# Kernel optimization log

Hardware: AMD Instinct MI355X
Metric: run time of the kernel (lower is better)

Reference implementation:

```python
import jax, jax.numpy as jnp
import numpy as np

CE_W, BOUND_W, DICE_W, SMOOTH = 1.0, 0.1, 1.0, 1e-6


def setup_inputs() -> dict:
    key = jax.random.key(0)
    k1, k2 = jax.random.split(key)
    B, C, H, W = 8, 1, 256, 256
    logits = jax.random.normal(k1, (B, C, H, W), dtype=jnp.float32)
    target = jax.random.uniform(k2, (B, C, H, W), dtype=jnp.float32)
    return {"logits": logits, "target": target}


def _edt(fg):
    # fg: [B, H, W] bool foreground mask. Returns exact Euclidean distance
    # transform of the background (0 at foreground), matching
    # scipy.ndimage.distance_transform_edt(1 - fg).
    B, H, W = fg.shape
    INF = jnp.float32(H + W)  # larger than any in-image 1D distance

    # --- pass 1: vertical distance to nearest foreground in each column ---
    fg_t = jnp.transpose(fg, (1, 0, 2))  # [H, B, W], scan over rows

    def step(carry, fg_row):
        d = jnp.where(fg_row, 0.0, carry + 1.0)
        return d, d

    init = jnp.full((B, W), INF, dtype=jnp.float32)
    _, g_fwd = jax.lax.scan(step, init, fg_t)                 # top-down
    _, g_bwd = jax.lax.scan(step, init, fg_t, reverse=True)   # bottom-up
    g = jnp.minimum(g_fwd, g_bwd)          # [H, B, W]
    g = jnp.transpose(g, (1, 0, 2))        # [B, H, W]

    # --- pass 2: exact squared EDT per row: min_k (j-k)^2 + g[i,k]^2 ---
    j = jnp.arange(W, dtype=jnp.float32)
    offs2 = (j[:, None] - j[None, :]) ** 2                    # [W, W]
    # [B, H, Wj, Wk] intermediate -> min over k
    dt2 = jnp.min(g[:, :, None, :] ** 2 + offs2[None, None, :, :], axis=-1)
    dt = jnp.sqrt(dt2)

    # empty masks get an all-zero distance map (scipy branch in the original)
    nonempty = jnp.any(fg, axis=(1, 2))
    return jnp.where(nonempty[:, None, None], dt, 0.0)


def reference(logits, target):
    target = jnp.clip(target.astype(jnp.float32), 0.0, 1.0)

    # BCEWithLogitsLoss (mean): stable log(1 + e^x) - x*t
    ce = jnp.mean(jnp.logaddexp(0.0, logits) - logits * target)

    probs = jnp.clip(jax.nn.sigmoid(logits), SMOOTH, 1.0 - SMOOTH)

    # Dice over flattened tensors
    p, t = probs.reshape(-1), target.reshape(-1)
    inter = jnp.sum(p * t)
    dice = 1.0 - (2.0 * inter + SMOOTH) / (jnp.sum(p) + jnp.sum(t) + SMOOTH)

    # Boundary: mean(probs * EDT(target > 0.5)) -- EDT is non-differentiable data
    fg = target[:, 0] > 0.5                      # [B, H, W]
    dt = jax.lax.stop_gradient(_edt(fg))[:, None]  # [B, 1, H, W]
    boundary = jnp.mean(probs * dt)

    total = CE_W * ce + DICE_W * dice + BOUND_W * boundary
    return total, ce, dice, boundary
```

## Files before the change

### kernel.cpp

```cpp
#include <hip/hip_runtime.h>

#define BB 8
#define HH 256
#define WW 256
#define NROWS (BB * HH)
#define NTOT (BB * HH * WW)

__global__ __launch_bounds__(256) void build_masks(
    const float* __restrict__ target, unsigned* __restrict__ masks) {
  const int s = blockIdx.x;
  const int b = blockIdx.y;
  const int j = threadIdx.x;
  const float* base = target + b * (HH * WW) + s * 32 * WW + j;
  unsigned m = 0;
#pragma unroll
  for (int r = 0; r < 32; ++r)
    if (base[r * WW] > 0.5f) m |= (1u << r);
  masks[b * 2048 + s * 256 + j] = m;
}

__global__ __launch_bounds__(256) void main_kernel(
    const float* __restrict__ logits, const float* __restrict__ target,
    const unsigned* __restrict__ masks,
    float* __restrict__ partials ) {
  __shared__ float s_g2[WW];
  __shared__ float s_red[4 * 5];
  __shared__ int s_any[4];
  __shared__ int s_rmax[4];

  const int row = blockIdx.x;
  const int b = row >> 8;
  const int i = row & 255;
  const int j = threadIdx.x;
  const int rowbase = row * WW;
  const int lane = j & 63;
  const int wave = j >> 6;

  unsigned m[8];
#pragma unroll
  for (int w = 0; w < 8; ++w) m[w] = masks[b * 2048 + w * 256 + j];

  const int wi = i >> 5, r = i & 31;
  int dUp = 1 << 30, dDn = 1 << 30;
  const unsigned cur = m[wi] >> r;
  if (cur) {
    dUp = __builtin_ctz(cur);
  } else {
    int off = 32 - r;
    for (int w2 = wi + 1; w2 < 8; ++w2, off += 32)
      if (m[w2]) { dUp = off + __builtin_ctz(m[w2]); break; }
  }
  const unsigned curd = m[wi] << (31 - r);
  if (curd) {
    dDn = __builtin_clz(curd);
  } else {
    int off = r + 1;
    for (int w2 = wi - 1; w2 >= 0; --w2, off += 32)
      if (m[w2]) { dDn = off + __builtin_clz(m[w2]); break; }
  }
  const int d = min(dUp, dDn);
  s_g2[j] = (d < 256) ? (float)(d * d) : 1.0e9f;
  const int rj = min(d, 255);

  const unsigned many = m[0] | m[1] | m[2] | m[3] | m[4] | m[5] | m[6] | m[7];
  const int wave_any = __any(many != 0u);
  int rmax = rj;
#pragma unroll
  for (int off = 32; off > 0; off >>= 1) rmax = max(rmax, __shfl_down(rmax, off, 64));
  if (lane == 0) { s_any[wave] = wave_any; s_rmax[wave] = rmax; }
  __syncthreads();
  const int nonempty = s_any[0] | s_any[1] | s_any[2] | s_any[3];
  const int R = max(max(s_rmax[0], s_rmax[1]), max(s_rmax[2], s_rmax[3]));

  float mn = 1.0e30f;
  for (int dlt = -R; dlt <= R; ++dlt) {
    const int k = j + dlt;
    if ((unsigned)k < 256u)
      mn = fminf(mn, (float)(dlt * dlt) + s_g2[k]);
  }
  const float dt = nonempty ? sqrtf(mn) : 0.0f;

  const float x = logits[rowbase + j];
  float t = target[rowbase + j];
  t = fminf(fmaxf(t, 0.0f), 1.0f);
  const float e = __expf(-fabsf(x));
  const float inv = 1.0f / (1.0f + e);
  const float ce = fmaxf(x, 0.0f) + __logf(1.0f + e) - x * t;
  float p = (x >= 0.0f) ? inv : e * inv;
  p = fminf(fmaxf(p, 1e-6f), 1.0f - 1e-6f);

  float v[5];
  v[0] = ce;
  v[1] = p;
  v[2] = t;
  v[3] = p * t;
  v[4] = p * dt;

#pragma unroll
  for (int q = 0; q < 5; ++q) {
    float s = v[q];
#pragma unroll
    for (int off = 32; off > 0; off >>= 1) s += __shfl_down(s, off, 64);
    if (lane == 0) s_red[wave * 5 + q] = s;
  }
  __syncthreads();
  if (j == 0) {
#pragma unroll
    for (int q = 0; q < 5; ++q) {
      const float s = s_red[q] + s_red[5 + q] + s_red[10 + q] + s_red[15 + q];
      partials[q * NROWS + row] = s;
    }
  }
}

__global__ __launch_bounds__(256) void finalize(
    const float* __restrict__ partials, float* __restrict__ out) {
  __shared__ double s_red[4 * 5];
  const int j = threadIdx.x;
  double acc[5] = {0.0, 0.0, 0.0, 0.0, 0.0};
  for (int i = j; i < NROWS; i += 256) {
#pragma unroll
    for (int q = 0; q < 5; ++q) acc[q] += (double)partials[q * NROWS + i];
  }
  const int lane = j & 63;
  const int wave = j >> 6;
#pragma unroll
  for (int q = 0; q < 5; ++q) {
    double s = acc[q];
#pragma unroll
    for (int off = 32; off > 0; off >>= 1) s += __shfl_down(s, off, 64);
    if (lane == 0) s_red[wave * 5 + q] = s;
  }
  __syncthreads();
  if (j == 0) {
    double sum[5];
#pragma unroll
    for (int q = 0; q < 5; ++q)
      sum[q] = s_red[q] + s_red[5 + q] + s_red[10 + q] + s_red[15 + q];
    const double n = (double)NTOT;
    const double ce = sum[0] / n;
    const double dice = 1.0 - (2.0 * sum[3] + 1e-6) / (sum[1] + sum[2] + 1e-6);
    const double boundary = sum[4] / n;
    const double total = 1.0 * ce + 1.0 * dice + 0.1 * boundary;
    out[0] = (float)total;
    out[1] = (float)ce;
    out[2] = (float)dice;
    out[3] = (float)boundary;
  }
}

extern "C" void kernel_launch(void* const* d_in, const int* in_sizes, int n_in,
                              void* d_out, int out_size, void* d_ws,
                              size_t ws_size, hipStream_t stream) {
  const float* logits = (const float*)d_in[0];
  const float* target = (const float*)d_in[1];
  float* out = (float*)d_out;

  char* ws = (char*)d_ws;
  unsigned* masks = (unsigned*)ws;
  float* partials = (float*)(ws + 64 * 1024);

  build_masks<<<dim3(8, 8), 256, 0, stream>>>(target, masks);
  main_kernel<<<NROWS, 256, 0, stream>>>(logits, target, masks, partials);
  finalize<<<1, 256, 0, stream>>>(partials, out);
}
```

Measured before the change: 69.09 us.

## Process four rows per block and fuse finalize via atomic last-block reduction

Each block now handles four rows of the same image, so the eight mask words are loaded once per four rows and the block-level reductions and syncs are amortised. The separate finalize kernel is removed: blocks atomically add double partials into a workspace accumulator and the last-arriving block computes the outputs. This saves a kernel launch and the partials round trip, but adds double atomics contention and makes the EDT search radius R the maximum over four rows.

```diff
diff --git a/kernel.cpp b/kernel.cpp
--- a/kernel.cpp
+++ b/kernel.cpp
@@ -3,14 +3,26 @@
 #define BB 8
 #define HH 256
 #define WW 256
-#define NROWS (BB * HH)
 #define NTOT (BB * HH * WW)
+#define RPB 4
+#define NBLK (BB * HH / RPB)
+
+struct Accum {
+  double s[5];
+  unsigned int count;
+};
 
 __global__ __launch_bounds__(256) void build_masks(
-    const float* __restrict__ target, unsigned* __restrict__ masks) {
+    const float* __restrict__ target, unsigned* __restrict__ masks,
+    Accum* __restrict__ acc) {
   const int s = blockIdx.x;
   const int b = blockIdx.y;
   const int j = threadIdx.x;
+  if (s == 0 && b == 0 && j == 0) {
+#pragma unroll
+    for (int q = 0; q < 5; ++q) acc->s[q] = 0.0;
+    acc->count = 0u;
+  }
   const float* base = target + b * (HH * WW) + s * 32 * WW + j;
   unsigned m = 0;
 #pragma unroll
@@ -21,81 +33,83 @@
 
 __global__ __launch_bounds__(256) void main_kernel(
     const float* __restrict__ logits, const float* __restrict__ target,
-    const unsigned* __restrict__ masks,
-    float* __restrict__ partials ) {
-  __shared__ float s_g2[WW];
+    const unsigned* __restrict__ masks, Accum* __restrict__ acc,
+    float* __restrict__ out) {
+  __shared__ float s_g2[RPB][WW];
   __shared__ float s_red[4 * 5];
-  __shared__ int s_any[4];
-  __shared__ int s_rmax[4];
+  __shared__ int s_im[4 * 2];
 
-  const int row = blockIdx.x;
-  const int b = row >> 8;
-  const int i = row & 255;
+  const int g = blockIdx.x;
+  const int b = g >> 6;
+  const int i0 = (g & 63) * RPB;
   const int j = threadIdx.x;
-  const int rowbase = row * WW;
-  const int lane = j & 63;
-  const int wave = j >> 6;
+  const int lane = j & 63, wave = j >> 6;
 
   unsigned m[8];
 #pragma unroll
   for (int w = 0; w < 8; ++w) m[w] = masks[b * 2048 + w * 256 + j];
+  const unsigned many = m[0] | m[1] | m[2] | m[3] | m[4] | m[5] | m[6] | m[7];
 
-  const int wi = i >> 5, r = i & 31;
-  int dUp = 1 << 30, dDn = 1 << 30;
-  const unsigned cur = m[wi] >> r;
-  if (cur) {
-    dUp = __builtin_ctz(cur);
-  } else {
-    int off = 32 - r;
-    for (int w2 = wi + 1; w2 < 8; ++w2, off += 32)
-      if (m[w2]) { dUp = off + __builtin_ctz(m[w2]); break; }
+  int rmax = 0;
+#pragma unroll
+  for (int r = 0; r < RPB; ++r) {
+    const int i = i0 + r;
+    const int wi = i >> 5, rr = i & 31;
+    int dUp = 1 << 30, dDn = 1 << 30;
+    const unsigned cur = m[wi] >> rr;
+    if (cur) {
+      dUp = __builtin_ctz(cur);
+    } else {
+      int off = 32 - rr;
+      for (int w2 = wi + 1; w2 < 8; ++w2, off += 32)
+        if (m[w2]) { dUp = off + __builtin_ctz(m[w2]); break; }
+    }
+    const unsigned curd = m[wi] << (31 - rr);
+    if (curd) {
+      dDn = __builtin_clz(curd);
+    } else {
+      int off = rr + 1;
+      for (int w2 = wi - 1; w2 >= 0; --w2, off += 32)
+        if (m[w2]) { dDn = off + __builtin_clz(m[w2]); break; }
+    }
+    const int d = min(dUp, dDn);
+    s_g2[r][j] = (d < 256) ? (float)(d * d) : 1.0e9f;
+    rmax = max(rmax, min(d, 255));
   }
-  const unsigned curd = m[wi] << (31 - r);
-  if (curd) {
-    dDn = __builtin_clz(curd);
-  } else {
-    int off = r + 1;
-    for (int w2 = wi - 1; w2 >= 0; --w2, off += 32)
-      if (m[w2]) { dDn = off + __builtin_clz(m[w2]); break; }
+
+  const int wave_any = __any(many != 0u);
+#pragma unroll
+  for (int off = 32; off > 0; off >>= 1)
+    rmax = max(rmax, __shfl_down(rmax, off, 64));
+  if (lane == 0) { s_im[wave * 2] = wave_any; s_im[wave * 2 + 1] = rmax; }
+  __syncthreads();
+  const int nonempty = s_im[0] | s_im[2] | s_im[4] | s_im[6];
+  const int R = max(max(s_im[1], s_im[3]), max(s_im[5], s_im[7]));
+
+  float v0 = 0.f, v1 = 0.f, v2 = 0.f, v3 = 0.f, v4 = 0.f;
+#pragma unroll
+  for (int r = 0; r < RPB; ++r) {
+    float mn = 1.0e30f;
+    for (int dlt = -R; dlt <= R; ++dlt) {
+      const int k = j + dlt;
+      if ((unsigned)k < 256u)
+        mn = fminf(mn, (float)(dlt * dlt) + s_g2[r][k]);
+    }
+    const float dt = nonempty ? sqrtf(mn) : 0.0f;
+
+    const int idx = (b * HH + i0 + r) * WW + j;
+    const float x = logits[idx];
+    float t = target[idx];
+    t = fminf(fmaxf(t, 0.0f), 1.0f);
+    const float e = __expf(-fabsf(x));
+    const float inv = 1.0f / (1.0f + e);
+    const float ce = fmaxf(x, 0.0f) + __logf(1.0f + e) - x * t;
+    float p = (x >= 0.0f) ? inv : e * inv;
+    p = fminf(fmaxf(p, 1e-6f), 1.0f - 1e-6f);
+    v0 += ce; v1 += p; v2 += t; v3 += p * t; v4 += p * dt;
   }
-  const int d = min(dUp, dDn);
-  s_g2[j] = (d < 256) ? (float)(d * d) : 1.0e9f;
-  const int rj = min(d, 255);
 
-  const unsigned many = m[0] | m[1] | m[2] | m[3] | m[4] | m[5] | m[6] | m[7];
-  const int wave_any = __any(many != 0u);
-  int rmax = rj;
-#pragma unroll
-  for (int off = 32; off > 0; off >>= 1) rmax = max(rmax, __shfl_down(rmax, off, 64));
-  if (lane == 0) { s_any[wave] = wave_any; s_rmax[wave] = rmax; }
-  __syncthreads();
-  const int nonempty = s_any[0] | s_any[1] | s_any[2] | s_any[3];
-  const int R = max(max(s_rmax[0], s_rmax[1]), max(s_rmax[2], s_rmax[3]));
-
-  float mn = 1.0e30f;
-  for (int dlt = -R; dlt <= R; ++dlt) {
-    const int k = j + dlt;
-    if ((unsigned)k < 256u)
-      mn = fminf(mn, (float)(dlt * dlt) + s_g2[k]);
-  }
-  const float dt = nonempty ? sqrtf(mn) : 0.0f;
-
-  const float x = logits[rowbase + j];
-  float t = target[rowbase + j];
-  t = fminf(fmaxf(t, 0.0f), 1.0f);
-  const float e = __expf(-fabsf(x));
-  const float inv = 1.0f / (1.0f + e);
-  const float ce = fmaxf(x, 0.0f) + __logf(1.0f + e) - x * t;
-  float p = (x >= 0.0f) ? inv : e * inv;
-  p = fminf(fmaxf(p, 1e-6f), 1.0f - 1e-6f);
-
-  float v[5];
-  v[0] = ce;
-  v[1] = p;
-  v[2] = t;
-  v[3] = p * t;
-  v[4] = p * dt;
-
+  float v[5] = {v0, v1, v2, v3, v4};
 #pragma unroll
   for (int q = 0; q < 5; ++q) {
     float s = v[q];
@@ -108,44 +122,25 @@
 #pragma unroll
     for (int q = 0; q < 5; ++q) {
       const float s = s_red[q] + s_red[5 + q] + s_red[10 + q] + s_red[15 + q];
-      partials[q * NROWS + row] = s;
+      atomicAdd(&acc->s[q], (double)s);
     }
-  }
-}
-
-__global__ __launch_bounds__(256) void finalize(
-    const float* __restrict__ partials, float* __restrict__ out) {
-  __shared__ double s_red[4 * 5];
-  const int j = threadIdx.x;
-  double acc[5] = {0.0, 0.0, 0.0, 0.0, 0.0};
-  for (int i = j; i < NROWS; i += 256) {
+    __threadfence();
+    const unsigned arrived = atomicAdd(&acc->count, 1u);
+    if (arrived == NBLK - 1) {
+      __threadfence();
+      double sum[5];
 #pragma unroll
-    for (int q = 0; q < 5; ++q) acc[q] += (double)partials[q * NROWS + i];
-  }
-  const int lane = j & 63;
-  const int wave = j >> 6;
-#pragma unroll
-  for (int q = 0; q < 5; ++q) {
-    double s = acc[q];
-#pragma unroll
-    for (int off = 32; off > 0; off >>= 1) s += __shfl_down(s, off, 64);
-    if (lane == 0) s_red[wave * 5 + q] = s;
-  }
-  __syncthreads();
-  if (j == 0) {
-    double sum[5];
-#pragma unroll
-    for (int q = 0; q < 5; ++q)
-      sum[q] = s_red[q] + s_red[5 + q] + s_red[10 + q] + s_red[15 + q];
-    const double n = (double)NTOT;
-    const double ce = sum[0] / n;
-    const double dice = 1.0 - (2.0 * sum[3] + 1e-6) / (sum[1] + sum[2] + 1e-6);
-    const double boundary = sum[4] / n;
-    const double total = 1.0 * ce + 1.0 * dice + 0.1 * boundary;
-    out[0] = (float)total;
-    out[1] = (float)ce;
-    out[2] = (float)dice;
-    out[3] = (float)boundary;
+      for (int q = 0; q < 5; ++q) sum[q] = atomicAdd(&acc->s[q], 0.0);
+      const double n = (double)NTOT;
+      const double ce = sum[0] / n;
+      const double dice =
+          1.0 - (2.0 * sum[3] + 1e-6) / (sum[1] + sum[2] + 1e-6);
+      const double boundary = sum[4] / n;
+      out[0] = (float)(ce + dice + 0.1 * boundary);
+      out[1] = (float)ce;
+      out[2] = (float)dice;
+      out[3] = (float)boundary;
+    }
   }
 }
 
@@ -158,9 +153,8 @@
 
   char* ws = (char*)d_ws;
   unsigned* masks = (unsigned*)ws;
-  float* partials = (float*)(ws + 64 * 1024);
+  Accum* acc = (Accum*)(ws + 64 * 1024);
 
-  build_masks<<<dim3(8, 8), 256, 0, stream>>>(target, masks);
-  main_kernel<<<NROWS, 256, 0, stream>>>(logits, target, masks, partials);
-  finalize<<<1, 256, 0, stream>>>(partials, out);
+  build_masks<<<dim3(8, 8), 256, 0, stream>>>(target, masks, acc);
+  main_kernel<<<NBLK, 256, 0, stream>>>(logits, target, masks, acc, out);
 }
```

Result: slower. 101.5 us (+46.9%).
